# Kernel tuning notes

Measured on AMD Instinct MI355X. Metric: run time of the kernel, lower is better.

## Reference

```python
import jax, jax.numpy as jnp
import numpy as np

B, T, HM = 2, 2048, 1024
HEADS = 16
DK = (HM // 2) // HEADS   # expand_k = 0.5 -> key_dim 512, per-head 32
DV = HM // HEADS          # expand_v = 1.0 -> per-head 64
LOW_RANK = 16             # gate low-rank dim (fla default)
GATE_NORM = 16.0          # gate_logit_normalizer (fla default)
EPS = 1e-5


def setup_inputs() -> dict:
    key = jax.random.key(0)
    ks = jax.random.split(key, 12)
    def p(k, shape, s=0.02):
        return jax.random.normal(k, shape, jnp.float32) * s
    return dict(
        x=jax.random.normal(ks[0], (B, T, HM), jnp.float32),
        ln_w=jnp.ones((HM,), jnp.float32), ln_b=jnp.zeros((HM,), jnp.float32),
        Wq=p(ks[1], (HM, HEADS * DK)), Wk=p(ks[2], (HM, HEADS * DK)),
        Wv=p(ks[3], (HM, HEADS * DV)),
        gk_w1=p(ks[4], (HM, LOW_RANK)), gk_w2=p(ks[5], (LOW_RANK, HEADS * DK)),
        gk_b2=jnp.zeros((HEADS * DK,), jnp.float32),
        Wg=p(ks[6], (HM, HEADS * DV)), rms_w=jnp.ones((DV,), jnp.float32),
        Wo=p(ks[7], (HEADS * DV, HM)),
        W1=p(ks[8], (HM, 2 * HM)), b1=jnp.zeros((2 * HM,), jnp.float32),
        W2=p(ks[9], (2 * HM, HM)), b2=jnp.zeros((HM,), jnp.float32),
    )


def _ln(x, w, b):
    m = x.mean(-1, keepdims=True)
    v = ((x - m) ** 2).mean(-1, keepdims=True)
    return (x - m) * jax.lax.rsqrt(v + EPS) * w + b


def _rms(x, w):
    return x * jax.lax.rsqrt((x * x).mean(-1, keepdims=True) + EPS) * w


def _gla(q, k, v, gk):
    # gated linear attention recurrence:
    # S_t = diag(exp(gk_t)) S_{t-1} + k_t v_t^T ;  o_t = q_t S_t
    # q,k,gk: [B,T,H,DK], v: [B,T,H,DV]
    def step(S, inp):
        qt, kt, vt, gt = inp
        S = jnp.exp(gt)[..., None] * S + kt[..., None] * vt[..., None, :]
        return S, jnp.einsum('bhk,bhkv->bhv', qt, S)
    xs = tuple(jnp.moveaxis(a, 1, 0) for a in (q, k, v, gk))
    S0 = jnp.zeros((q.shape[0], q.shape[2], q.shape[3], v.shape[3]), q.dtype)
    _, o = jax.lax.scan(step, S0, xs)
    return jnp.moveaxis(o, 0, 1)


def reference(x, ln_w, ln_b, Wq, Wk, Wv, gk_w1, gk_w2, gk_b2, Wg, rms_w, Wo, W1, b1, W2, b2):
    Bb, Tt, _ = x.shape
    h = _ln(x, ln_w, ln_b)
    q = (h @ Wq).reshape(Bb, Tt, HEADS, DK)
    k = (h @ Wk).reshape(Bb, Tt, HEADS, DK)
    v = (h @ Wv).reshape(Bb, Tt, HEADS, DV)
    gk = (jax.nn.log_sigmoid((h @ gk_w1) @ gk_w2 + gk_b2) / GATE_NORM)
    gk = gk.reshape(Bb, Tt, HEADS, DK)
    o = _gla(q * (DK ** -0.5), k, v, gk)
    # output gate: RMSNorm(o) * swish(g)  (FusedRMSNormSwishGate)
    g = (h @ Wg).reshape(Bb, Tt, HEADS, DV)
    o = _rms(o, rms_w) * (g * jax.nn.sigmoid(g))
    x = x + o.reshape(Bb, Tt, HEADS * DV) @ Wo
    h2 = _ln(x, ln_w, ln_b)  # same shared norm module
    return x + jax.nn.gelu(h2 @ W1 + b1, approximate=False) @ W2 + b2
```

## Files before the change

kernel.cpp:

```cpp
#include <hip/hip_runtime.h>
#include <hip/hip_bf16.h>
#include <math.h>


using bf16 = __hip_bfloat16;
typedef __attribute__((ext_vector_type(8))) short bf16x8;
typedef __attribute__((ext_vector_type(4))) float f32x4;

#define BT 4096
#define HM 1024
#define DK 32
#define DV 64
#define NC 32
#define CHK 64

#if defined(__has_builtin)
#if __has_builtin(__builtin_amdgcn_global_load_lds)
#define HAVE_GLDS 1
#endif
#endif

#ifdef HAVE_GLDS
#define GLDS16(g, l) __builtin_amdgcn_global_load_lds( \
    (const __attribute__((address_space(1))) unsigned int*)(g), \
    (__attribute__((address_space(3))) unsigned int*)(l), 16, 0, 0)
#else
#define GLDS16(g, l) (*(int4*)(l) = *(const int4*)(g))
#endif

__device__ __forceinline__ float b2f(bf16 v) { return __bfloat162float(v); }
__device__ __forceinline__ bf16 f2b(float v) { return __float2bfloat16(v); }
__device__ __forceinline__ float clampf(float v, float lim) {
    return fminf(fmaxf(v, -lim), lim);
}
__device__ __forceinline__ float lo16(unsigned int u) {
    union { unsigned int i; float f; } c; c.i = u << 16; return c.f;
}
__device__ __forceinline__ float hi16(unsigned int u) {
    union { unsigned int i; float f; } c; c.i = u & 0xffff0000u; return c.f;
}
__device__ __forceinline__ void acc8(float a, uint4 r, float* o) {
    o[0] += a * lo16(r.x); o[1] += a * hi16(r.x);
    o[2] += a * lo16(r.y); o[3] += a * hi16(r.y);
    o[4] += a * lo16(r.z); o[5] += a * hi16(r.z);
    o[6] += a * lo16(r.w); o[7] += a * hi16(r.w);
}

__global__ __launch_bounds__(256) void detect_dtype(
    const unsigned int* __restrict__ x, int* __restrict__ flag)
{
    int tid = threadIdx.x;
    int cnt = 0;
    for (int i = 0; i < 16; ++i) {
        unsigned int w = x[tid * 16 + i];
        unsigned int e_lo = (w >> 7) & 0xffu;
        unsigned int e_hi = (w >> 23) & 0xffu;
        cnt += (e_lo >= 110 && e_lo <= 135 && e_hi >= 110 && e_hi <= 135) ? 1 : 0;
    }
    __shared__ int red[256];
    red[tid] = cnt;
    __syncthreads();
    for (int s = 128; s > 0; s >>= 1) {
        if (tid < s) red[tid] += red[tid + s];
        __syncthreads();
    }
    if (tid == 0) *flag = (red[0] > 2048) ? 1 : 0;
}

struct SmallCvt { const void* s[8]; bf16* d[8]; int n[8]; };
__global__ __launch_bounds__(256) void cvt_small(SmallCvt sc, const int* __restrict__ flag)
{
    bool isb = (*flag != 0);
    int stride = gridDim.x * 256;
    #pragma unroll
    for (int seg = 0; seg < 8; ++seg) {
        int n = sc.n[seg];
        for (int i = blockIdx.x * 256 + threadIdx.x; i < n; i += stride) {
            if (isb) ((ushort*)sc.d[seg])[i] = ((const ushort*)sc.s[seg])[i];
            else     sc.d[seg][i] = f2b(((const float*)sc.s[seg])[i]);
        }
    }
}

struct TDesc { const void* src; ushort* dst; int R, C, tile0; };
struct TAll { TDesc d[7]; };
__global__ __launch_bounds__(256) void transpose_all(
    TAll ta, const int* __restrict__ flag)
{
    bool isb = (*flag != 0);
    int bid = blockIdx.x;
    int seg = 0;
    #pragma unroll
    for (int i = 1; i < 7; ++i) if (bid >= ta.d[i].tile0) seg = i;
    const void* src = ta.d[seg].src;
    ushort* dst = ta.d[seg].dst;
    int R = ta.d[seg].R, C = ta.d[seg].C;
    int t = bid - ta.d[seg].tile0;
    int tilesX = C >> 5;
    int c0 = (t % tilesX) * 32, r0 = (t / tilesX) * 32;

    __shared__ ushort tile[32][33];
    int x = threadIdx.x, y = threadIdx.y;
    #pragma unroll
    for (int dy = 0; dy < 32; dy += 8) {
        size_t idx = (size_t)(r0 + y + dy) * C + c0 + x;
        ushort v;
        if (isb) v = ((const ushort*)src)[idx];
        else { bf16 tb = f2b(((const float*)src)[idx]); v = *(ushort*)&tb; }
        tile[y + dy][x] = v;
    }
    __syncthreads();
    #pragma unroll
    for (int dy = 0; dy < 32; dy += 8)
        dst[(size_t)(c0 + y + dy) * R + r0 + x] = tile[x][y + dy];
}

template <int DO_GK>
__global__ __launch_bounds__(256) void ln_kernel(
    const void* __restrict__ x, const bf16* __restrict__ w, const bf16* __restrict__ b,
    bf16* __restrict__ out, const int* __restrict__ flag, int force,
    const bf16* __restrict__ w1, const bf16* __restrict__ w2,
    const bf16* __restrict__ b2i, bf16* __restrict__ gkout)
{
    bool isb = (force >= 0) ? (force != 0) : (*flag != 0);
    size_t base = (size_t)blockIdx.x * HM;
    int tid = threadIdx.x;
    float v[4], s = 0.f, s2 = 0.f;
    #pragma unroll
    for (int u = 0; u < 4; ++u) {
        size_t idx = base + tid + u * 256;
        float f = isb ? b2f(((const bf16*)x)[idx]) : ((const float*)x)[idx];
        v[u] = f; s += f; s2 += f * f;
    }
    #pragma unroll
    for (int off = 32; off >= 1; off >>= 1) {
        s  += __shfl_down(s, off);
        s2 += __shfl_down(s2, off);
    }
    __shared__ float ra[4], rb[4];
    __shared__ float hrow[1024];
    int wave = tid >> 6;
    if ((tid & 63) == 0) { ra[wave] = s; rb[wave] = s2; }
    __syncthreads();
    s = ra[0] + ra[1] + ra[2] + ra[3];
    s2 = rb[0] + rb[1] + rb[2] + rb[3];
    float mean = s * (1.f / HM);
    float var = fmaxf(s2 * (1.f / HM) - mean * mean, 0.f);
    float rs = rsqrtf(var + 1e-5f);
    #pragma unroll
    for (int u = 0; u < 4; ++u) {
        int col = tid + u * 256;
        float h = (v[u] - mean) * rs * b2f(w[col]) + b2f(b[col]);
        out[base + col] = f2b(h);
        if constexpr (DO_GK) hrow[col] = h;
    }
    if constexpr (DO_GK) {
        __syncthreads();
        int d = tid & 15, seg = tid >> 4;
        float sg = 0.f;
        #pragma unroll 8
        for (int j = 0; j < 64; ++j) {
            int i = seg * 64 + j;
            sg += hrow[i] * b2f(w1[i * 16 + d]);
        }
        __shared__ float red[256];
        __shared__ float g1[16];
        red[tid] = sg;
        __syncthreads();
        if (tid < 16) {
            float t = 0.f;
            #pragma unroll
            for (int s2i = 0; s2i < 16; ++s2i) t += red[s2i * 16 + tid];
            g1[tid] = t;
        }
        __syncthreads();
        #pragma unroll
        for (int rep = 0; rep < 2; ++rep) {
            int n = tid + rep * 256;
            float z = b2f(b2i[n]);
            #pragma unroll
            for (int r = 0; r < 16; ++r) z += g1[r] * b2f(w2[r * 512 + n]);
            z = clampf(z, 30.f);
            float ls = (z >= 0.f) ? -log1pf(expf(-z)) : (z - log1pf(expf(z)));
            gkout[blockIdx.x * 512 + n] = f2b(ls * 0.0625f);
        }
    }
}

template <int MODE>
__global__ __launch_bounds__(256) void gemm128(
    const bf16* __restrict__ A, const bf16* __restrict__ Wt,
    const bf16* __restrict__ bias, void* __restrict__ out, int M, int N, int K)
{
    __shared__ __align__(16) ushort As[128 * 64];
    __shared__ __align__(16) ushort Bs[128 * 64];
    int tid = threadIdx.x;
    int w = tid >> 6, l = tid & 63;
    int bm = blockIdx.x * 128, bn = blockIdx.y * 128;
    int row16 = l & 15, quad = l >> 4;

    const ushort* Au = (const ushort*)A;
    const ushort* Wu = (const ushort*)Wt;

    int ab = (w >> 1) * 4;
    int bb = (w & 1) * 4;

    f32x4 acc[4][4] = {};
    for (int k0 = 0; k0 < K; k0 += 64) {
        #pragma unroll
        for (int p = 0; p < 2; ++p) {
            #pragma unroll
            for (int i = 0; i < 2; ++i) {
                int j = i * 4 + w;
                const ushort* gA = Au + (size_t)(bm + j * 16 + row16) * K
                                   + k0 + p * 32 + quad * 8;
                GLDS16(gA, &As[p * 4096 + j * 512 + l * 8]);
                const ushort* gB = Wu + (size_t)(bn + j * 16 + row16) * K
                                   + k0 + p * 32 + quad * 8;
                GLDS16(gB, &Bs[p * 4096 + j * 512 + l * 8]);
            }
        }
        __syncthreads();
        #pragma unroll
        for (int p = 0; p < 2; ++p) {
            int fo = p * 4096 + quad * 128 + row16 * 8;
            bf16x8 af[4], bw[4];
            #pragma unroll
            for (int mi = 0; mi < 4; ++mi) af[mi] = *(const bf16x8*)&As[(ab + mi) * 512 + fo];
            #pragma unroll
            for (int ni = 0; ni < 4; ++ni) bw[ni] = *(const bf16x8*)&Bs[(bb + ni) * 512 + fo];
            #pragma unroll
            for (int mi = 0; mi < 4; ++mi)
                #pragma unroll
                for (int ni = 0; ni < 4; ++ni)
                    acc[mi][ni] = __builtin_amdgcn_mfma_f32_16x16x32_bf16(af[mi], bw[ni], acc[mi][ni], 0, 0, 0);
        }
        __syncthreads();
    }
    #pragma unroll
    for (int mi = 0; mi < 4; ++mi) {
        #pragma unroll
        for (int ni = 0; ni < 4; ++ni) {
            int col = bn + (w & 1) * 64 + ni * 16 + row16;
            #pragma unroll
            for (int r = 0; r < 4; ++r) {
                int row = bm + (w >> 1) * 64 + mi * 16 + quad * 4 + r;
                size_t idx = (size_t)row * N + col;
                float v = acc[mi][ni][r];
                if constexpr (MODE == 0) {
                    ((bf16*)out)[idx] = f2b(clampf(v, 1e4f));
                } else {
                    float t = clampf(v + b2f(bias[col]), 50.f);
                    ((bf16*)out)[idx] = f2b(0.5f * t * (1.f + erff(t * 0.70710678f)));
                }
            }
        }
    }
}

template <int MODE>
__global__ __launch_bounds__(256) void gemm_bt(
    const bf16* __restrict__ A, const bf16* __restrict__ Wt,
    const bf16* __restrict__ bias, const void* __restrict__ resid,
    void* __restrict__ out, int M, int N, int K, const int* __restrict__ oflag)
{
    __shared__ __align__(16) ushort As[128 * 64];
    __shared__ __align__(16) ushort Bs[64 * 64];
    int tid = threadIdx.x;
    int w = tid >> 6, l = tid & 63;
    int bm = blockIdx.x * 128, bn = blockIdx.y * 64;
    int row16 = l & 15, quad = l >> 4;
    bool isb = (*oflag != 0);

    const ushort* Au = (const ushort*)A;
    const ushort* Wu = (const ushort*)Wt;

    f32x4 acc[4][2] = {};
    for (int k0 = 0; k0 < K; k0 += 64) {
        #pragma unroll
        for (int i = 0; i < 4; ++i) {
            int j = i * 4 + w;
            const ushort* g = Au + (size_t)(bm + (j >> 1) * 16 + row16) * K
                              + k0 + (j & 1) * 32 + quad * 8;
            GLDS16(g, &As[j * 512 + l * 8]);
        }
        #pragma unroll
        for (int i = 0; i < 2; ++i) {
            int j = i * 4 + w;
            const ushort* g = Wu + (size_t)(bn + (j >> 1) * 16 + row16) * K
                              + k0 + (j & 1) * 32 + quad * 8;
            GLDS16(g, &Bs[j * 512 + l * 8]);
        }
        __syncthreads();
        #pragma unroll
        for (int s = 0; s < 2; ++s) {
            int fo = (s * 4 + quad) * 128 + row16 * 8;
            bf16x8 af[4], bw[2];
            #pragma unroll
            for (int mi = 0; mi < 4; ++mi)
                af[mi] = *(const bf16x8*)&As[((w >> 1) * 4 + mi) * 1024 + fo];
            #pragma unroll
            for (int ni = 0; ni < 2; ++ni)
                bw[ni] = *(const bf16x8*)&Bs[((w & 1) * 2 + ni) * 1024 + fo];
            #pragma unroll
            for (int mi = 0; mi < 4; ++mi)
                #pragma unroll
                for (int ni = 0; ni < 2; ++ni)
                    acc[mi][ni] = __builtin_amdgcn_mfma_f32_16x16x32_bf16(af[mi], bw[ni], acc[mi][ni], 0, 0, 0);
        }
        __syncthreads();
    }
    #pragma unroll
    for (int mi = 0; mi < 4; ++mi) {
        #pragma unroll
        for (int ni = 0; ni < 2; ++ni) {
            int col = bn + (w & 1) * 32 + ni * 16 + row16;
            #pragma unroll
            for (int r = 0; r < 4; ++r) {
                int row = bm + (w >> 1) * 64 + mi * 16 + quad * 4 + r;
                size_t idx = (size_t)row * N + col;
                float v = acc[mi][ni][r];
                if constexpr (MODE == 1) {
                    float rv = isb ? b2f(((const bf16*)resid)[idx])
                                   : ((const float*)resid)[idx];
                    ((float*)out)[idx] = clampf(rv + v, 1e5f);
                } else {
                    float t = clampf(v + b2f(bias[col]) + ((const float*)resid)[idx], 2e5f);
                    if (isb) ((bf16*)out)[idx] = f2b(t);
                    else     ((float*)out)[idx] = t;
                }
            }
        }
    }
}

__global__ __launch_bounds__(256) void gla_phase1(
    const bf16* __restrict__ gkb, const bf16* __restrict__ qvg,
    float* __restrict__ clbuf, float* __restrict__ Dbuf, float* __restrict__ Pbuf)
{
    int bh = blockIdx.x, c = blockIdx.y;
    int b = bh >> 4, hh = bh & 15;
    int row0 = b * 2048 + c * CHK;
    __shared__ float glog[CHK][DK + 1];
    __shared__ float wk[CHK][DK + 1];
    __shared__ float segsum[8][DK + 1];
    __shared__ __align__(16) ushort vt[CHK][DV];
    int tid = threadIdx.x;
    int k = tid & 31, i8 = (tid >> 5) * 8;
    int seg = tid >> 5;
    #pragma unroll
    for (int u = 0; u < 8; ++u) {
        int i = i8 + u;
        float g = b2f(gkb[(size_t)(row0 + i) * 512 + hh * 32 + k]);
        glog[i][k] = fminf(fmaxf(g, -2.f), 0.f);
    }
    {
        int cc = tid & 7, ii = tid >> 3;
        #pragma unroll
        for (int h = 0; h < 2; ++h) {
            int i = ii + h * 32;
            uint4 val = *(const uint4*)((const ushort*)qvg + (size_t)(row0 + i) * 3072 + 1024 + hh * 64 + cc * 8);
            *(uint4*)&vt[i][cc * 8] = val;
        }
    }
    __syncthreads();
    {
        float run = 0.f;
        #pragma unroll
        for (int u = 0; u < 8; ++u) {
            run += glog[i8 + u][k];
            glog[i8 + u][k] = run;
        }
        segsum[seg][k] = run;
    }
    __syncthreads();
    {
        float off = 0.f;
        for (int s = 0; s < seg; ++s) off += segsum[s][k];
        #pragma unroll
        for (int u = 0; u < 8; ++u) glog[i8 + u][k] += off;
    }
    __syncthreads();
    #pragma unroll
    for (int u = 0; u < 8; ++u) {
        int i = i8 + u;
        float cl = glog[i][k];
        float cl63 = glog[CHK - 1][k];
        clbuf[(size_t)(row0 + i) * 512 + hh * 32 + k] = cl;
        wk[i][k] = expf(fmaxf(cl63 - cl, -60.f)) *
            b2f(qvg[(size_t)(row0 + i) * 3072 + 512 + hh * 32 + k]);
    }
    if (tid < 32) Dbuf[(size_t)(bh * 32 + c) * 32 + tid] = expf(glog[CHK - 1][tid]);
    __syncthreads();
    int kk = tid >> 3, v8 = (tid & 7) * 8;
    float acc[8] = {};
    for (int j = 0; j < CHK; ++j) {
        float w = wk[j][kk];
        uint4 raw = *(const uint4*)&vt[j][v8];
        acc8(w, raw, acc);
    }
    float* Pp = Pbuf + (size_t)(bh * 32 + c) * 2048 + kk * 64 + v8;
    #pragma unroll
    for (int u = 0; u < 8; ++u) Pp[u] = acc[u];
}

__global__ __launch_bounds__(256) void gla_scan(
    const float* __restrict__ Pbuf, const float* __restrict__ Dbuf,
    float* __restrict__ Sbuf)
{
    int bh = blockIdx.x >> 3, vg8 = blockIdx.x & 7;
    int kk = threadIdx.x >> 3, vv = vg8 * 8 + (threadIdx.x & 7);
    float S = 0.f;
    for (int c = 0; c < NC; ++c) {
        size_t idx = (size_t)(bh * 32 + c) * 2048 + kk * 64 + vv;
        float P = Pbuf[idx];
        float D = Dbuf[(size_t)(bh * 32 + c) * 32 + kk];
        Sbuf[idx] = S;
        S = D * S + P;
    }
}

__global__ __launch_bounds__(256) void gla_phase3(
    const bf16* __restrict__ qvg,
    const float* __restrict__ clbuf, const float* __restrict__ Sbuf,
    const bf16* __restrict__ rmsw, bf16* __restrict__ obuf)
{
    int bh = blockIdx.x, c = blockIdx.y;
    int b = bh >> 4, hh = bh & 15;
    int row0 = b * 2048 + c * CHK;
    __shared__ float qs[CHK][36], ks[CHK][36];
    __shared__ float S0[DK][68];
    __shared__ float Amat[CHK][CHK + 1];
    __shared__ __align__(16) ushort vt[CHK][DV];
    int tid = threadIdx.x;
    {
        int k = tid & 31, i8 = (tid >> 5) * 8;
        #pragma unroll
        for (int u = 0; u < 8; ++u) {
            int i = i8 + u;
            size_t r = (size_t)(row0 + i);
            int col = hh * 32 + k;
            float cl = fmaxf(clbuf[r * 512 + col], -60.f);
            qs[i][k] = b2f(qvg[r * 3072 + col]) * expf(cl) * 0.17677669529663687f;
            ks[i][k] = b2f(qvg[r * 3072 + 512 + col]) * expf(-cl);
        }
    }
    {
        int cc = tid & 7, ii = tid >> 3;
        #pragma unroll
        for (int h = 0; h < 2; ++h) {
            int i = ii + h * 32;
            uint4 val = *(const uint4*)((const ushort*)qvg + (size_t)(row0 + i) * 3072 + 1024 + hh * 64 + cc * 8);
            *(uint4*)&vt[i][cc * 8] = val;
        }
    }
    {
        int kk = tid >> 3, v8 = (tid & 7) * 8;
        const float* Sp = Sbuf + (size_t)(bh * 32 + c) * 2048 + kk * 64 + v8;
        *(f32x4*)&S0[kk][v8]     = *(const f32x4*)Sp;
        *(f32x4*)&S0[kk][v8 + 4] = *(const f32x4*)(Sp + 4);
    }
    __syncthreads();
    int i = tid >> 2, jb = tid & 3;
    for (int jj = 0; jj < 16; ++jj) {
        int j = jb + jj * 4;
        float d = 0.f;
        if (j <= i) {
            const f32x4* qp = (const f32x4*)qs[i];
            const f32x4* kp = (const f32x4*)ks[j];
            #pragma unroll
            for (int q8 = 0; q8 < 8; ++q8) {
                f32x4 a = qp[q8], bq = kp[q8];
                d += a.x * bq.x + a.y * bq.y + a.z * bq.z + a.w * bq.w;
            }
        }
        Amat[i][j] = d;
    }
    __syncthreads();
    float o[16] = {};
    int vv = jb * 16;
    for (int j = 0; j < CHK; ++j) {
        float a = Amat[i][j];
        uint4 r0 = *(const uint4*)&vt[j][vv];
        uint4 r1 = *(const uint4*)&vt[j][vv + 8];
        acc8(a, r0, o);
        acc8(a, r1, o + 8);
    }
    #pragma unroll
    for (int kk = 0; kk < DK; ++kk) {
        float qv = qs[i][kk];
        const f32x4* Sp = (const f32x4*)&S0[kk][vv];
        #pragma unroll
        for (int q4 = 0; q4 < 4; ++q4) {
            f32x4 sv = Sp[q4];
            o[q4 * 4 + 0] += qv * sv.x; o[q4 * 4 + 1] += qv * sv.y;
            o[q4 * 4 + 2] += qv * sv.z; o[q4 * 4 + 3] += qv * sv.w;
        }
    }
    float ss = 0.f;
    #pragma unroll
    for (int u = 0; u < 16; ++u) ss += o[u] * o[u];
    ss += __shfl_xor(ss, 1);
    ss += __shfl_xor(ss, 2);
    float sc = rsqrtf(fmaxf(ss, 0.f) * (1.f / DV) + 1e-5f);
    size_t r = (size_t)(row0 + i);
    #pragma unroll
    for (int u = 0; u < 16; ++u) {
        float g = b2f(qvg[r * 3072 + 2048 + hh * 64 + vv + u]);
        float sw = g / (1.f + expf(-g));
        obuf[r * 1024 + hh * 64 + vv + u] = f2b(clampf(o[u] * sc * b2f(rmsw[vv + u]) * sw, 3e4f));
    }
}

extern "C" void kernel_launch(void* const* d_in, const int* in_sizes, int n_in,
                              void* d_out, int out_size, void* d_ws, size_t ws_size,
                              hipStream_t stream) {
    (void)in_sizes; (void)n_in; (void)out_size; (void)ws_size;

    char* ws = (char*)d_ws;
    const size_t MB = 1024 * 1024;
    const size_t KB = 1024;
    bf16*  WqkT = (bf16*)(ws + 0);
    bf16*  WkT  = (bf16*)(ws + 1 * MB);
    bf16*  WvgT = (bf16*)(ws + 2 * MB);
    bf16*  WgT  = (bf16*)(ws + 4 * MB);
    bf16*  WoT  = (bf16*)(ws + 6 * MB);
    bf16*  W1T  = (bf16*)(ws + 8 * MB);
    bf16*  W2T  = (bf16*)(ws + 12 * MB);
    bf16*  hbuf = (bf16*)(ws + 16 * MB);
    bf16*  qvg  = (bf16*)(ws + 24 * MB);
    bf16*  gkb  = (bf16*)(ws + 48 * MB);
    float* clbf = (float*)(ws + 52 * MB);
    float* Dbuf = (float*)(ws + 60 * MB);
    float* Pbuf = (float*)(ws + 61 * MB);
    float* Sbuf = (float*)(ws + 69 * MB);
    bf16*  obuf = (bf16*)(ws + 61 * MB);
    float* ybuf = (float*)(ws + 32 * MB);
    bf16*  f1   = (bf16*)(ws + 48 * MB);
    bf16*  clnw = (bf16*)(ws + 85 * MB);
    bf16*  clnb = (bf16*)(ws + 85 * MB + 64 * KB);
    bf16*  cgw1 = (bf16*)(ws + 85 * MB + 128 * KB);
    bf16*  cgw2 = (bf16*)(ws + 85 * MB + 192 * KB);
    bf16*  cgb2 = (bf16*)(ws + 85 * MB + 256 * KB);
    bf16*  crms = (bf16*)(ws + 85 * MB + 320 * KB);
    bf16*  cb1  = (bf16*)(ws + 85 * MB + 384 * KB);
    bf16*  cb2  = (bf16*)(ws + 85 * MB + 448 * KB);
    int*   flag = (int*)(ws + 85 * MB + 512 * KB);

    hipLaunchKernelGGL(detect_dtype, dim3(1), dim3(256), 0, stream,
                       (const unsigned int*)d_in[0], flag);

    SmallCvt sc;
    sc.s[0] = d_in[1];  sc.d[0] = clnw; sc.n[0] = 1024;
    sc.s[1] = d_in[2];  sc.d[1] = clnb; sc.n[1] = 1024;
    sc.s[2] = d_in[6];  sc.d[2] = cgw1; sc.n[2] = 16384;
    sc.s[3] = d_in[7];  sc.d[3] = cgw2; sc.n[3] = 8192;
    sc.s[4] = d_in[8];  sc.d[4] = cgb2; sc.n[4] = 512;
    sc.s[5] = d_in[10]; sc.d[5] = crms; sc.n[5] = 64;
    sc.s[6] = d_in[13]; sc.d[6] = cb1;  sc.n[6] = 2048;
    sc.s[7] = d_in[15]; sc.d[7] = cb2;  sc.n[7] = 1024;
    hipLaunchKernelGGL(cvt_small, dim3(64), dim3(256), 0, stream, sc, flag);

    TAll ta;
    ta.d[0] = { d_in[3],  (ushort*)WqkT, 1024, 512,  0 };
    ta.d[1] = { d_in[4],  (ushort*)WkT,  1024, 512,  512 };
    ta.d[2] = { d_in[5],  (ushort*)WvgT, 1024, 1024, 1024 };
    ta.d[3] = { d_in[9],  (ushort*)WgT,  1024, 1024, 2048 };
    ta.d[4] = { d_in[11], (ushort*)WoT,  1024, 1024, 3072 };
    ta.d[5] = { d_in[12], (ushort*)W1T,  1024, 2048, 4096 };
    ta.d[6] = { d_in[14], (ushort*)W2T,  2048, 1024, 6144 };
    hipLaunchKernelGGL(transpose_all, dim3(8192), dim3(32, 8), 0, stream, ta, flag);

    hipLaunchKernelGGL((ln_kernel<1>), dim3(BT), dim3(256), 0, stream,
                       d_in[0], clnw, clnb, hbuf, (const int*)flag, -1,
                       cgw1, cgw2, cgb2, gkb);

    hipLaunchKernelGGL((gemm128<0>), dim3(32, 24), dim3(256), 0, stream,
                       hbuf, WqkT, (const bf16*)nullptr, (void*)qvg, BT, 3072, 1024);

    hipLaunchKernelGGL(gla_phase1, dim3(32, 32), dim3(256), 0, stream, gkb, qvg, clbf, Dbuf, Pbuf);
    hipLaunchKernelGGL(gla_scan, dim3(256), dim3(256), 0, stream, Pbuf, Dbuf, Sbuf);
    hipLaunchKernelGGL(gla_phase3, dim3(32, 32), dim3(256), 0, stream, qvg, clbf, Sbuf, crms, obuf);

    hipLaunchKernelGGL((gemm_bt<1>), dim3(32, 16), dim3(256), 0, stream,
                       obuf, WoT, (const bf16*)nullptr, (const void*)d_in[0], (void*)ybuf, BT, 1024, 1024, flag);
    hipLaunchKernelGGL((ln_kernel<0>), dim3(BT), dim3(256), 0, stream,
                       (const void*)ybuf, clnw, clnb, hbuf, (const int*)flag, 0,
                       (const bf16*)nullptr, (const bf16*)nullptr, (const bf16*)nullptr, (bf16*)nullptr);
    hipLaunchKernelGGL((gemm128<2>), dim3(32, 16), dim3(256), 0, stream,
                       hbuf, W1T, cb1, (void*)f1, BT, 2048, 1024);
    hipLaunchKernelGGL((gemm_bt<3>), dim3(32, 16), dim3(256), 0, stream,
                       f1, W2T, cb2, (const void*)ybuf, d_out, BT, 1024, 2048, flag);
}
```

Before: 404.3 us.

## Replace GEMM kernels with 256-row, 8-wave, double-buffered swizzled LDS pipeline

Replaces the two GEMM kernels with one templated kernel. It uses 512 threads and 256xBN output tiles, and double-buffers global-to-LDS loads two k-tiles ahead, interleaved with four MFMA quarter-steps. An XOR swizzle on LDS columns avoids bank conflicts, and s_setprio raises priority around the MFMA bursts. The goal is to hide memory latency and raise data reuse per block. The cost is far fewer blocks, as few as 128 for the N=1024 GEMMs, and large dynamic LDS use, which may leave many CUs idle.

```diff
diff --git a/kernel.cpp b/kernel.cpp
--- a/kernel.cpp
+++ b/kernel.cpp
@@ -187,140 +187,130 @@
     }
 }
 
-template <int MODE>
-__global__ __launch_bounds__(256) void gemm128(
-    const bf16* __restrict__ A, const bf16* __restrict__ Wt,
-    const bf16* __restrict__ bias, void* __restrict__ out, int M, int N, int K)
-{
-    __shared__ __align__(16) ushort As[128 * 64];
-    __shared__ __align__(16) ushort Bs[128 * 64];
-    int tid = threadIdx.x;
-    int w = tid >> 6, l = tid & 63;
-    int bm = blockIdx.x * 128, bn = blockIdx.y * 128;
-    int row16 = l & 15, quad = l >> 4;
-
-    const ushort* Au = (const ushort*)A;
-    const ushort* Wu = (const ushort*)Wt;
-
-    int ab = (w >> 1) * 4;
-    int bb = (w & 1) * 4;
-
-    f32x4 acc[4][4] = {};
-    for (int k0 = 0; k0 < K; k0 += 64) {
-        #pragma unroll
-        for (int p = 0; p < 2; ++p) {
-            #pragma unroll
-            for (int i = 0; i < 2; ++i) {
-                int j = i * 4 + w;
-                const ushort* gA = Au + (size_t)(bm + j * 16 + row16) * K
-                                   + k0 + p * 32 + quad * 8;
-                GLDS16(gA, &As[p * 4096 + j * 512 + l * 8]);
-                const ushort* gB = Wu + (size_t)(bn + j * 16 + row16) * K
-                                   + k0 + p * 32 + quad * 8;
-                GLDS16(gB, &Bs[p * 4096 + j * 512 + l * 8]);
-            }
-        }
-        __syncthreads();
-        #pragma unroll
-        for (int p = 0; p < 2; ++p) {
-            int fo = p * 4096 + quad * 128 + row16 * 8;
-            bf16x8 af[4], bw[4];
-            #pragma unroll
-            for (int mi = 0; mi < 4; ++mi) af[mi] = *(const bf16x8*)&As[(ab + mi) * 512 + fo];
-            #pragma unroll
-            for (int ni = 0; ni < 4; ++ni) bw[ni] = *(const bf16x8*)&Bs[(bb + ni) * 512 + fo];
-            #pragma unroll
-            for (int mi = 0; mi < 4; ++mi)
-                #pragma unroll
-                for (int ni = 0; ni < 4; ++ni)
-                    acc[mi][ni] = __builtin_amdgcn_mfma_f32_16x16x32_bf16(af[mi], bw[ni], acc[mi][ni], 0, 0, 0);
-        }
-        __syncthreads();
-    }
-    #pragma unroll
-    for (int mi = 0; mi < 4; ++mi) {
-        #pragma unroll
-        for (int ni = 0; ni < 4; ++ni) {
-            int col = bn + (w & 1) * 64 + ni * 16 + row16;
-            #pragma unroll
-            for (int r = 0; r < 4; ++r) {
-                int row = bm + (w >> 1) * 64 + mi * 16 + quad * 4 + r;
-                size_t idx = (size_t)row * N + col;
-                float v = acc[mi][ni][r];
-                if constexpr (MODE == 0) {
-                    ((bf16*)out)[idx] = f2b(clampf(v, 1e4f));
-                } else {
-                    float t = clampf(v + b2f(bias[col]), 50.f);
-                    ((bf16*)out)[idx] = f2b(0.5f * t * (1.f + erff(t * 0.70710678f)));
-                }
-            }
-        }
-    }
-}
-
-template <int MODE>
-__global__ __launch_bounds__(256) void gemm_bt(
+template <int BN, int MODE>
+__global__ __launch_bounds__(512, 2) void gemm8p(
     const bf16* __restrict__ A, const bf16* __restrict__ Wt,
     const bf16* __restrict__ bias, const void* __restrict__ resid,
     void* __restrict__ out, int M, int N, int K, const int* __restrict__ oflag)
 {
-    __shared__ __align__(16) ushort As[128 * 64];
-    __shared__ __align__(16) ushort Bs[64 * 64];
+    constexpr int NFRAG  = BN / 128;
+    constexpr int BLOADS = (BN == 256) ? 2 : 1;
+
+    extern __shared__ ushort sm[];
+    ushort* smA = sm;
+    ushort* smB = sm + 32768;
+
     int tid = threadIdx.x;
-    int w = tid >> 6, l = tid & 63;
-    int bm = blockIdx.x * 128, bn = blockIdx.y * 64;
-    int row16 = l & 15, quad = l >> 4;
-    bool isb = (*oflag != 0);
+    int wid = tid >> 6, l = tid & 63;
+    int wm = wid >> 2, wn = wid & 3;
+    int r16 = l & 15, quad = l >> 4;
+    int bm = blockIdx.x * 256, bn = blockIdx.y * BN;
+    bool isb = false;
+    if constexpr (MODE == 1 || MODE == 3) isb = (*oflag != 0);
 
     const ushort* Au = (const ushort*)A;
     const ushort* Wu = (const ushort*)Wt;
-
-    f32x4 acc[4][2] = {};
-    for (int k0 = 0; k0 < K; k0 += 64) {
-        #pragma unroll
-        for (int i = 0; i < 4; ++i) {
-            int j = i * 4 + w;
-            const ushort* g = Au + (size_t)(bm + (j >> 1) * 16 + row16) * K
-                              + k0 + (j & 1) * 32 + quad * 8;
-            GLDS16(g, &As[j * 512 + l * 8]);
-        }
+    const int NT = K >> 6;
+
+    auto stageA = [&](int t, int h) {
         #pragma unroll
         for (int i = 0; i < 2; ++i) {
-            int j = i * 4 + w;
-            const ushort* g = Wu + (size_t)(bn + (j >> 1) * 16 + row16) * K
-                              + k0 + (j & 1) * 32 + quad * 8;
-            GLDS16(g, &Bs[j * 512 + l * 8]);
-        }
-        __syncthreads();
-        #pragma unroll
-        for (int s = 0; s < 2; ++s) {
-            int fo = (s * 4 + quad) * 128 + row16 * 8;
-            bf16x8 af[4], bw[2];
-            #pragma unroll
-            for (int mi = 0; mi < 4; ++mi)
-                af[mi] = *(const bf16x8*)&As[((w >> 1) * 4 + mi) * 1024 + fo];
-            #pragma unroll
-            for (int ni = 0; ni < 2; ++ni)
-                bw[ni] = *(const bf16x8*)&Bs[((w & 1) * 2 + ni) * 1024 + fo];
-            #pragma unroll
-            for (int mi = 0; mi < 4; ++mi)
+            int j = i * 512 + tid;
+            int lr = j >> 3, slot = j & 7;
+            int r = (lr & 63) + h * 64 + (lr >> 6) * 128;
+            int sl = slot ^ (r & 7);
+            const ushort* g = Au + (size_t)(bm + r) * K + t * 64 + sl * 8;
+            GLDS16(g, &smA[(t & 1) * 16384 + r * 64 + slot * 8]);
+        }
+    };
+    auto stageB = [&](int t, int h) {
+        #pragma unroll
+        for (int i = 0; i < BLOADS; ++i) {
+            int j = i * 512 + tid;
+            int lr = j >> 3, slot = j & 7;
+            int r = (BN == 256) ? ((lr & 31) + h * 32 + (lr >> 5) * 64)
+                                : ((lr & 15) + h * 16 + (lr >> 4) * 32);
+            int sl = slot ^ (r & 7);
+            const ushort* g = Wu + (size_t)(bn + r) * K + t * 64 + sl * 8;
+            GLDS16(g, &smB[(t & 1) * (BN * 64) + r * 64 + slot * 8]);
+        }
+    };
+
+    int colx0 = (quad * 8) ^ ((r16 & 7) * 8);
+    int colx1 = colx0 ^ 32;
+
+    f32x4 acc[8][BN / 64] = {};
+
+    stageA(0, 0); stageB(0, 0); stageA(0, 1); stageB(0, 1);
+    if (NT > 1) { stageA(1, 0); stageB(1, 1); }
+    if constexpr (BN == 256) asm volatile("s_waitcnt vmcnt(4)" ::: "memory");
+    else                     asm volatile("s_waitcnt vmcnt(3)" ::: "memory");
+    __builtin_amdgcn_s_barrier();
+
+    for (int t = 0; t < NT; ++t) {
+        const int abase = (t & 1) * 16384;
+        const int bbase = (t & 1) * (BN * 64);
+        #pragma unroll
+        for (int q = 0; q < 4; ++q) {
+            const int mh = q >> 1;
+            const int nh = (q == 1 || q == 2) ? 1 : 0;
+            bf16x8 af[2][4], bw[2][NFRAG];
+            #pragma unroll
+            for (int mf = 0; mf < 4; ++mf) {
+                int r = wm * 128 + mh * 64 + mf * 16 + r16;
+                af[0][mf] = *(const bf16x8*)&smA[abase + r * 64 + colx0];
+                af[1][mf] = *(const bf16x8*)&smA[abase + r * 64 + colx1];
+            }
+            #pragma unroll
+            for (int nf = 0; nf < NFRAG; ++nf) {
+                int r = wn * (BN / 4) + nh * (NFRAG * 16) + nf * 16 + r16;
+                bw[0][nf] = *(const bf16x8*)&smB[bbase + r * 64 + colx0];
+                bw[1][nf] = *(const bf16x8*)&smB[bbase + r * 64 + colx1];
+            }
+            if (q == 0) { if (t + 1 < NT) stageA(t + 1, 1); }
+            if (q == 1) { if (t + 1 < NT) stageB(t + 1, 0); }
+            if (q == 2) { if (t + 2 < NT) stageA(t + 2, 0); }
+            if (q == 3) { if (t + 2 < NT) stageB(t + 2, 1); }
+            __builtin_amdgcn_s_barrier();
+            asm volatile("s_waitcnt lgkmcnt(0)" ::: "memory");
+            __builtin_amdgcn_s_setprio(1);
+            #pragma unroll
+            for (int mf = 0; mf < 4; ++mf)
                 #pragma unroll
-                for (int ni = 0; ni < 2; ++ni)
-                    acc[mi][ni] = __builtin_amdgcn_mfma_f32_16x16x32_bf16(af[mi], bw[ni], acc[mi][ni], 0, 0, 0);
-        }
-        __syncthreads();
-    }
-    #pragma unroll
-    for (int mi = 0; mi < 4; ++mi) {
-        #pragma unroll
-        for (int ni = 0; ni < 2; ++ni) {
-            int col = bn + (w & 1) * 32 + ni * 16 + row16;
+                for (int nf = 0; nf < NFRAG; ++nf) {
+                    f32x4& a = acc[mh * 4 + mf][nh * NFRAG + nf];
+                    a = __builtin_amdgcn_mfma_f32_16x16x32_bf16(af[0][mf], bw[0][nf], a, 0, 0, 0);
+                    a = __builtin_amdgcn_mfma_f32_16x16x32_bf16(af[1][mf], bw[1][nf], a, 0, 0, 0);
+                }
+            __builtin_amdgcn_s_setprio(0);
+            if (q == 3) {
+                if (t + 2 < NT) {
+                    if constexpr (BN == 256) asm volatile("s_waitcnt vmcnt(4)" ::: "memory");
+                    else                     asm volatile("s_waitcnt vmcnt(3)" ::: "memory");
+                } else {
+                    asm volatile("s_waitcnt vmcnt(0)" ::: "memory");
+                }
+            }
+            __builtin_amdgcn_s_barrier();
+        }
+    }
+
+    #pragma unroll
+    for (int am = 0; am < 8; ++am) {
+        int row0 = bm + wm * 128 + am * 16 + quad * 4;
+        #pragma unroll
+        for (int an = 0; an < BN / 64; ++an) {
+            int col = bn + wn * (BN / 4) + an * 16 + r16;
             #pragma unroll
             for (int r = 0; r < 4; ++r) {
-                int row = bm + (w >> 1) * 64 + mi * 16 + quad * 4 + r;
-                size_t idx = (size_t)row * N + col;
-                float v = acc[mi][ni][r];
-                if constexpr (MODE == 1) {
+                size_t idx = (size_t)(row0 + r) * N + col;
+                float v = acc[am][an][r];
+                if constexpr (MODE == 0) {
+                    ((bf16*)out)[idx] = f2b(clampf(v, 1e4f));
+                } else if constexpr (MODE == 2) {
+                    float t = clampf(v + b2f(bias[col]), 50.f);
+                    ((bf16*)out)[idx] = f2b(0.5f * t * (1.f + erff(t * 0.70710678f)));
+                } else if constexpr (MODE == 1) {
                     float rv = isb ? b2f(((const bf16*)resid)[idx])
                                    : ((const float*)resid)[idx];
                     ((float*)out)[idx] = clampf(rv + v, 1e5f);
@@ -575,20 +565,22 @@
                        d_in[0], clnw, clnb, hbuf, (const int*)flag, -1,
                        cgw1, cgw2, cgb2, gkb);
 
-    hipLaunchKernelGGL((gemm128<0>), dim3(32, 24), dim3(256), 0, stream,
-                       hbuf, WqkT, (const bf16*)nullptr, (void*)qvg, BT, 3072, 1024);
+    hipLaunchKernelGGL((gemm8p<256, 0>), dim3(16, 12), dim3(512), 131072, stream,
+                       hbuf, WqkT, (const bf16*)nullptr, nullptr, (void*)qvg,
+                       BT, 3072, 1024, flag);
 
     hipLaunchKernelGGL(gla_phase1, dim3(32, 32), dim3(256), 0, stream, gkb, qvg, clbf, Dbuf, Pbuf);
     hipLaunchKernelGGL(gla_scan, dim3(256), dim3(256), 0, stream, Pbuf, Dbuf, Sbuf);
     hipLaunchKernelGGL(gla_phase3, dim3(32, 32), dim3(256), 0, stream, qvg, clbf, Sbuf, crms, obuf);
 
-    hipLaunchKernelGGL((gemm_bt<1>), dim3(32, 16), dim3(256), 0, stream,
-                       obuf, WoT, (const bf16*)nullptr, (const void*)d_in[0], (void*)ybuf, BT, 1024, 1024, flag);
+    hipLaunchKernelGGL((gemm8p<128, 1>), dim3(16, 8), dim3(512), 98304, stream,
+                       obuf, WoT, (const bf16*)nullptr, (const void*)d_in[0], (void*)ybuf,
+                       BT, 1024, 1024, flag);
     hipLaunchKernelGGL((ln_kernel<0>), dim3(BT), dim3(256), 0, stream,
                        (const void*)ybuf, clnw, clnb, hbuf, (const int*)flag, 0,
                        (const bf16*)nullptr, (const bf16*)nullptr, (const bf16*)nullptr, (bf16*)nullptr);
-    hipLaunchKernelGGL((gemm128<2>), dim3(32, 16), dim3(256), 0, stream,
-                       hbuf, W1T, cb1, (void*)f1, BT, 2048, 1024);
-    hipLaunchKernelGGL((gemm_bt<3>), dim3(32, 16), dim3(256), 0, stream,
+    hipLaunchKernelGGL((gemm8p<128, 2>), dim3(16, 16), dim3(512), 98304, stream,
+                       hbuf, W1T, cb1, nullptr, (void*)f1, BT, 2048, 1024, flag);
+    hipLaunchKernelGGL((gemm8p<128, 3>), dim3(16, 8), dim3(512), 98304, stream,
                        f1, W2T, cb2, (const void*)ybuf, d_out, BT, 1024, 2048, flag);
 }
```

New measurement: 396.6 us. Within noise of the previous version (-1.9%).

## Double-buffer LDS tiles in both GEMM kernels to overlap loads with MFMA

Applied to the files above, without the earlier changes.

Both GEMM kernels now use two LDS buffers per operand and ping-pong between them. The next K-tile is issued with global_load_lds while MFMAs run on the current tile, with one explicit vmcnt wait and barrier per stage. This targets the exposed global-load latency of the single-buffered loop. It doubles LDS use (64KB per block for gemm128), which may lower occupancy. The loop assumes an even tile count or relies on the guards, and sched_barrier limits compiler reordering.

```diff
diff --git a/kernel.cpp b/kernel.cpp
--- a/kernel.cpp
+++ b/kernel.cpp
@@ -192,8 +192,10 @@
     const bf16* __restrict__ A, const bf16* __restrict__ Wt,
     const bf16* __restrict__ bias, void* __restrict__ out, int M, int N, int K)
 {
-    __shared__ __align__(16) ushort As[128 * 64];
-    __shared__ __align__(16) ushort Bs[128 * 64];
+    __shared__ __align__(16) ushort As0[128 * 64];
+    __shared__ __align__(16) ushort Bs0[128 * 64];
+    __shared__ __align__(16) ushort As1[128 * 64];
+    __shared__ __align__(16) ushort Bs1[128 * 64];
     int tid = threadIdx.x;
     int w = tid >> 6, l = tid & 63;
     int bm = blockIdx.x * 128, bn = blockIdx.y * 128;
@@ -204,39 +206,60 @@
 
     int ab = (w >> 1) * 4;
     int bb = (w & 1) * 4;
+    const int NT = K >> 6;
 
     f32x4 acc[4][4] = {};
-    for (int k0 = 0; k0 < K; k0 += 64) {
-        #pragma unroll
-        for (int p = 0; p < 2; ++p) {
-            #pragma unroll
-            for (int i = 0; i < 2; ++i) {
-                int j = i * 4 + w;
-                const ushort* gA = Au + (size_t)(bm + j * 16 + row16) * K
-                                   + k0 + p * 32 + quad * 8;
-                GLDS16(gA, &As[p * 4096 + j * 512 + l * 8]);
-                const ushort* gB = Wu + (size_t)(bn + j * 16 + row16) * K
-                                   + k0 + p * 32 + quad * 8;
-                GLDS16(gB, &Bs[p * 4096 + j * 512 + l * 8]);
-            }
-        }
-        __syncthreads();
-        #pragma unroll
-        for (int p = 0; p < 2; ++p) {
-            int fo = p * 4096 + quad * 128 + row16 * 8;
-            bf16x8 af[4], bw[4];
-            #pragma unroll
-            for (int mi = 0; mi < 4; ++mi) af[mi] = *(const bf16x8*)&As[(ab + mi) * 512 + fo];
-            #pragma unroll
-            for (int ni = 0; ni < 4; ++ni) bw[ni] = *(const bf16x8*)&Bs[(bb + ni) * 512 + fo];
-            #pragma unroll
-            for (int mi = 0; mi < 4; ++mi)
-                #pragma unroll
-                for (int ni = 0; ni < 4; ++ni)
-                    acc[mi][ni] = __builtin_amdgcn_mfma_f32_16x16x32_bf16(af[mi], bw[ni], acc[mi][ni], 0, 0, 0);
-        }
-        __syncthreads();
-    }
+
+#define STAGE128(k0, As, Bs) do { \
+    _Pragma("unroll") \
+    for (int p = 0; p < 2; ++p) { \
+        _Pragma("unroll") \
+        for (int i = 0; i < 2; ++i) { \
+            int j = i * 4 + w; \
+            const ushort* gA = Au + (size_t)(bm + j * 16 + row16) * K \
+                               + (k0) + p * 32 + quad * 8; \
+            GLDS16(gA, &As[p * 4096 + j * 512 + l * 8]); \
+            const ushort* gB = Wu + (size_t)(bn + j * 16 + row16) * K \
+                               + (k0) + p * 32 + quad * 8; \
+            GLDS16(gB, &Bs[p * 4096 + j * 512 + l * 8]); \
+        } \
+    } } while (0)
+
+#define COMP128(As, Bs) do { \
+    _Pragma("unroll") \
+    for (int p = 0; p < 2; ++p) { \
+        int fo = p * 4096 + quad * 128 + row16 * 8; \
+        bf16x8 af[4], bwv[4]; \
+        _Pragma("unroll") \
+        for (int mi = 0; mi < 4; ++mi) af[mi] = *(const bf16x8*)&As[(ab + mi) * 512 + fo]; \
+        _Pragma("unroll") \
+        for (int ni = 0; ni < 4; ++ni) bwv[ni] = *(const bf16x8*)&Bs[(bb + ni) * 512 + fo]; \
+        _Pragma("unroll") \
+        for (int mi = 0; mi < 4; ++mi) \
+            _Pragma("unroll") \
+            for (int ni = 0; ni < 4; ++ni) \
+                acc[mi][ni] = __builtin_amdgcn_mfma_f32_16x16x32_bf16(af[mi], bwv[ni], acc[mi][ni], 0, 0, 0); \
+    } } while (0)
+
+    STAGE128(0, As0, Bs0);
+    asm volatile("s_waitcnt vmcnt(0)" ::: "memory");
+    __builtin_amdgcn_s_barrier();
+    __builtin_amdgcn_sched_barrier(0);
+    for (int t = 0; t < NT; t += 2) {
+        if (t + 1 < NT) STAGE128((t + 1) * 64, As1, Bs1);
+        COMP128(As0, Bs0);
+        asm volatile("s_waitcnt vmcnt(0)" ::: "memory");
+        __builtin_amdgcn_s_barrier();
+        __builtin_amdgcn_sched_barrier(0);
+        if (t + 2 < NT) STAGE128((t + 2) * 64, As0, Bs0);
+        COMP128(As1, Bs1);
+        asm volatile("s_waitcnt vmcnt(0)" ::: "memory");
+        __builtin_amdgcn_s_barrier();
+        __builtin_amdgcn_sched_barrier(0);
+    }
+#undef STAGE128
+#undef COMP128
+
     #pragma unroll
     for (int mi = 0; mi < 4; ++mi) {
         #pragma unroll
@@ -264,8 +287,10 @@
     const bf16* __restrict__ bias, const void* __restrict__ resid,
     void* __restrict__ out, int M, int N, int K, const int* __restrict__ oflag)
 {
-    __shared__ __align__(16) ushort As[128 * 64];
-    __shared__ __align__(16) ushort Bs[64 * 64];
+    __shared__ __align__(16) ushort As0[128 * 64];
+    __shared__ __align__(16) ushort Bs0[64 * 64];
+    __shared__ __align__(16) ushort As1[128 * 64];
+    __shared__ __align__(16) ushort Bs1[64 * 64];
     int tid = threadIdx.x;
     int w = tid >> 6, l = tid & 63;
     int bm = blockIdx.x * 128, bn = blockIdx.y * 64;
@@ -274,42 +299,63 @@
 
     const ushort* Au = (const ushort*)A;
     const ushort* Wu = (const ushort*)Wt;
+    const int NT = K >> 6;
 
     f32x4 acc[4][2] = {};
-    for (int k0 = 0; k0 < K; k0 += 64) {
-        #pragma unroll
-        for (int i = 0; i < 4; ++i) {
-            int j = i * 4 + w;
-            const ushort* g = Au + (size_t)(bm + (j >> 1) * 16 + row16) * K
-                              + k0 + (j & 1) * 32 + quad * 8;
-            GLDS16(g, &As[j * 512 + l * 8]);
-        }
-        #pragma unroll
-        for (int i = 0; i < 2; ++i) {
-            int j = i * 4 + w;
-            const ushort* g = Wu + (size_t)(bn + (j >> 1) * 16 + row16) * K
-                              + k0 + (j & 1) * 32 + quad * 8;
-            GLDS16(g, &Bs[j * 512 + l * 8]);
-        }
-        __syncthreads();
-        #pragma unroll
-        for (int s = 0; s < 2; ++s) {
-            int fo = (s * 4 + quad) * 128 + row16 * 8;
-            bf16x8 af[4], bw[2];
-            #pragma unroll
-            for (int mi = 0; mi < 4; ++mi)
-                af[mi] = *(const bf16x8*)&As[((w >> 1) * 4 + mi) * 1024 + fo];
-            #pragma unroll
-            for (int ni = 0; ni < 2; ++ni)
-                bw[ni] = *(const bf16x8*)&Bs[((w & 1) * 2 + ni) * 1024 + fo];
-            #pragma unroll
-            for (int mi = 0; mi < 4; ++mi)
-                #pragma unroll
-                for (int ni = 0; ni < 2; ++ni)
-                    acc[mi][ni] = __builtin_amdgcn_mfma_f32_16x16x32_bf16(af[mi], bw[ni], acc[mi][ni], 0, 0, 0);
-        }
-        __syncthreads();
-    }
+
+#define STAGEBT(k0, As, Bs) do { \
+    _Pragma("unroll") \
+    for (int i = 0; i < 4; ++i) { \
+        int j = i * 4 + w; \
+        const ushort* g = Au + (size_t)(bm + (j >> 1) * 16 + row16) * K \
+                          + (k0) + (j & 1) * 32 + quad * 8; \
+        GLDS16(g, &As[j * 512 + l * 8]); \
+    } \
+    _Pragma("unroll") \
+    for (int i = 0; i < 2; ++i) { \
+        int j = i * 4 + w; \
+        const ushort* g = Wu + (size_t)(bn + (j >> 1) * 16 + row16) * K \
+                          + (k0) + (j & 1) * 32 + quad * 8; \
+        GLDS16(g, &Bs[j * 512 + l * 8]); \
+    } } while (0)
+
+#define COMPBT(As, Bs) do { \
+    _Pragma("unroll") \
+    for (int s = 0; s < 2; ++s) { \
+        int fo = (s * 4 + quad) * 128 + row16 * 8; \
+        bf16x8 af[4], bwv[2]; \
+        _Pragma("unroll") \
+        for (int mi = 0; mi < 4; ++mi) \
+            af[mi] = *(const bf16x8*)&As[((w >> 1) * 4 + mi) * 1024 + fo]; \
+        _Pragma("unroll") \
+        for (int ni = 0; ni < 2; ++ni) \
+            bwv[ni] = *(const bf16x8*)&Bs[((w & 1) * 2 + ni) * 1024 + fo]; \
+        _Pragma("unroll") \
+        for (int mi = 0; mi < 4; ++mi) \
+            _Pragma("unroll") \
+            for (int ni = 0; ni < 2; ++ni) \
+                acc[mi][ni] = __builtin_amdgcn_mfma_f32_16x16x32_bf16(af[mi], bwv[ni], acc[mi][ni], 0, 0, 0); \
+    } } while (0)
+
+    STAGEBT(0, As0, Bs0);
+    asm volatile("s_waitcnt vmcnt(0)" ::: "memory");
+    __builtin_amdgcn_s_barrier();
+    __builtin_amdgcn_sched_barrier(0);
+    for (int t = 0; t < NT; t += 2) {
+        if (t + 1 < NT) STAGEBT((t + 1) * 64, As1, Bs1);
+        COMPBT(As0, Bs0);
+        asm volatile("s_waitcnt vmcnt(0)" ::: "memory");
+        __builtin_amdgcn_s_barrier();
+        __builtin_amdgcn_sched_barrier(0);
+        if (t + 2 < NT) STAGEBT((t + 2) * 64, As0, Bs0);
+        COMPBT(As1, Bs1);
+        asm volatile("s_waitcnt vmcnt(0)" ::: "memory");
+        __builtin_amdgcn_s_barrier();
+        __builtin_amdgcn_sched_barrier(0);
+    }
+#undef STAGEBT
+#undef COMPBT
+
     #pragma unroll
     for (int mi = 0; mi < 4; ++mi) {
         #pragma unroll
```

Measured after the change: 507.9 us. +25.6%, slower.
